# Optimization experiments

Measured on AMD Instinct MI355X. Metric: run time of the kernel, lower is better.

The kernel has to match this reference:

```python
import jax, jax.numpy as jnp
import numpy as np

E = 16        # n_routed_experts
D = 2048      # in_features
H = 1024      # d_intermediate per routed expert
K = 4         # n_activated_experts
SH = 1024     # shared expert hidden = n_shared_experts * d_intermediate
T = 2048      # tokens


def gated_mlp(x, w1, w2):
    # fc1 -> chunk -> y * silu(gate) -> fc2   (bias-free, as in mamba GatedMLP)
    y = x @ w1.T                      # [T, 2h]
    y, gate = jnp.split(y, 2, axis=-1)
    return (y * jax.nn.silu(gate)) @ w2.T


def setup_inputs() -> dict:
    key = jax.random.key(0)
    ks = jax.random.split(key, 6)
    s = 0.02  # init scale so softmax scores are well-behaved
    return {
        "x": jax.random.normal(ks[0], (T, D), jnp.float32),
        "gate_w": jax.random.normal(ks[1], (E, D), jnp.float32) * s,
        "w1": jax.random.normal(ks[2], (E, 2 * H, D), jnp.float32) * s,
        "w2": jax.random.normal(ks[3], (E, D, H), jnp.float32) * s,
        "sw1": jax.random.normal(ks[4], (2 * SH, D), jnp.float32) * s,
        "sw2": jax.random.normal(ks[5], (D, SH), jnp.float32) * s,
    }


def reference(x, gate_w, w1, w2, sw1, sw2):
    # ---- Gate (softmax scores in fp32, no bias, single expert group) ----
    scores = jax.nn.softmax((x @ gate_w.T).astype(jnp.float32), axis=-1)  # [T, E]
    top_vals, top_idx = jax.lax.top_k(scores, K)                          # [T, K]
    weights = top_vals.astype(x.dtype)  # route_scale = 1.0

    # Per-token routing weight per expert, [T, E]. topk indices are distinct
    # per token, matching `z[idx] += expert(x[idx]) * weights[idx, top]`.
    t_idx = jnp.arange(x.shape[0])[:, None]
    tok_w = jnp.zeros((x.shape[0], E), x.dtype).at[t_idx, top_idx].add(weights)

    # ---- Routed experts: accumulate weighted expert outputs ----
    def body(z, ew):
        w1_e, w2_e, we = ew  # [2H,D], [D,H], [T]
        return z + gated_mlp(x, w1_e, w2_e) * we[:, None], None

    z, _ = jax.lax.scan(body, jnp.zeros_like(x), (w1, w2, tok_w.T))

    # ---- Shared expert added to all tokens ----
    return z + gated_mlp(x, sw1, sw2)
```

## Files before the change

### kernel.cpp

```cpp
#include <hip/hip_runtime.h>
#include <stdint.h>

#define T_TOK 2048
#define D_IN  2048
#define H_I   1024
#define NE    16
#define TOPK  4
#define TWOH  2048
#define MAX_SLOTS 12288
#define MAX_TILES 96

typedef __attribute__((ext_vector_type(8))) __bf16 bf16x8;
typedef __attribute__((ext_vector_type(4))) float  f32x4;

__device__ __forceinline__ unsigned short f2bf(float f) {
  unsigned u = __float_as_uint(f);
  u += 0x7FFF + ((u >> 16) & 1);
  return (unsigned short)(u >> 16);
}
__device__ __forceinline__ float bf2f(unsigned short s) {
  return __uint_as_float(((unsigned)s) << 16);
}

__device__ __forceinline__ void group_meta(const int* __restrict__ cnt, int g,
                                           int& base, int& pc, int& shared_base) {
  int o = 0; base = 0; pc = T_TOK;
  for (int e = 0; e < NE; ++e) {
    int pce = (cnt[e] + 127) & ~127;
    if (e == g) { base = o; pc = pce; }
    o += pce;
  }
  shared_base = o;
  if (g == 16) base = o;
}

#define GLDS16(gp, lp) __builtin_amdgcn_global_load_lds( \
    (__attribute__((address_space(1))) void*)(gp),       \
    (__attribute__((address_space(3))) void*)(lp), 16, 0, 0)

#define R_X   1048576
#define R_W1  (R_X + 16777216)
#define R_W2  (R_W1 + 8388608)
#define R_SW1 (R_W2 + 1048576)
#define R_SW2 (R_SW1 + 524288)
__global__ void cvt_all(const float4* __restrict__ x,  const float4* __restrict__ w1,
                        const float4* __restrict__ w2, const float4* __restrict__ sw1,
                        const float4* __restrict__ sw2,
                        ushort4* __restrict__ xd,  ushort4* __restrict__ w1d,
                        ushort4* __restrict__ w2d, ushort4* __restrict__ sw1d,
                        ushort4* __restrict__ sw2d, int* __restrict__ cnt) {
  int i = blockIdx.x * 256 + threadIdx.x;
  if (i < NE) cnt[i] = 0;
  const float4* s; ushort4* d; int j;
  if      (i < R_X)   { s = x;   d = xd;   j = i; }
  else if (i < R_W1)  { s = w1;  d = w1d;  j = i - R_X; }
  else if (i < R_W2)  { s = w2;  d = w2d;  j = i - R_W1; }
  else if (i < R_SW1) { s = sw1; d = sw1d; j = i - R_W2; }
  else if (i < R_SW2) { s = sw2; d = sw2d; j = i - R_SW1; }
  else return;
  float4 f = s[j];
  ushort4 u;
  u.x = f2bf(f.x); u.y = f2bf(f.y); u.z = f2bf(f.z); u.w = f2bf(f.w);
  d[j] = u;
}

__global__ __launch_bounds__(256) void gate_topk(
    const float* __restrict__ x, const float* __restrict__ gw,
    int* __restrict__ cnt, int* __restrict__ cap_tok, float* __restrict__ cap_w,
    int* __restrict__ tk_ep)
{
  int t = blockIdx.x;
  const float* xr = x + (size_t)t * D_IN;
  float acc[NE];
#pragma unroll
  for (int e = 0; e < NE; ++e) acc[e] = 0.f;
  for (int d = threadIdx.x; d < D_IN; d += 256) {
    float xv = xr[d];
#pragma unroll
    for (int e = 0; e < NE; ++e) acc[e] += xv * gw[e * D_IN + d];
  }
#pragma unroll
  for (int e = 0; e < NE; ++e) {
    float v = acc[e];
#pragma unroll
    for (int o = 32; o > 0; o >>= 1) v += __shfl_down(v, o, 64);
    acc[e] = v;
  }
  __shared__ float red[4][NE];
  int wv = threadIdx.x >> 6, ln = threadIdx.x & 63;
  if (ln == 0) {
#pragma unroll
    for (int e = 0; e < NE; ++e) red[wv][e] = acc[e];
  }
  __syncthreads();
  if (threadIdx.x == 0) {
    float lg[NE];
    float mx = -1e30f;
#pragma unroll
    for (int e = 0; e < NE; ++e) {
      lg[e] = red[0][e] + red[1][e] + red[2][e] + red[3][e];
      mx = fmaxf(mx, lg[e]);
    }
    float s = 0.f;
#pragma unroll
    for (int e = 0; e < NE; ++e) { lg[e] = __expf(lg[e] - mx); s += lg[e]; }
    float inv = 1.f / s;
    bool used[NE] = {};
    for (int k = 0; k < TOPK; ++k) {
      float best = -1.f; int bi = 0;
      for (int e = 0; e < NE; ++e)
        if (!used[e] && lg[e] > best) { best = lg[e]; bi = e; }
      used[bi] = true;
      int pos = atomicAdd(&cnt[bi], 1);
      cap_tok[bi * T_TOK + pos] = t;
      cap_w[bi * T_TOK + pos]   = best * inv;
      tk_ep[t * TOPK + k] = (bi << 16) | pos;
    }
  }
}

__global__ void compact_lists(const int* __restrict__ cnt,
                              const int* __restrict__ cap_tok, const float* __restrict__ cap_w,
                              const int* __restrict__ tk_ep,
                              int* __restrict__ stok, float* __restrict__ swt,
                              int* __restrict__ tok2slot, int* __restrict__ tmap)
{
  int idx = blockIdx.x * 256 + threadIdx.x;
  if (idx == 0) {
    int k = 0, o = 0;
    for (int e = 0; e < NE; ++e) {
      int pce = (cnt[e] + 127) & ~127;
      for (int m = 0; m * 128 < pce && k < MAX_TILES; ++m)
        tmap[k++] = (e << 16) | (o + m * 128);
      o += pce;
    }
    for (int m = 0; m < 16 && k < MAX_TILES; ++m)
      tmap[k++] = (16 << 16) | (o + m * 128);
    tmap[MAX_TILES] = k;
  }
  if (idx < NE * T_TOK) {
    int e = idx >> 11, pos = idx & (T_TOK - 1);
    int base, pc, sb;
    group_meta(cnt, e, base, pc, sb);
    if (pos < pc) {
      int dst = base + pos;
      if (pos < cnt[e]) { stok[dst] = cap_tok[idx]; swt[dst] = cap_w[idx]; }
      else              { stok[dst] = 0;            swt[dst] = 0.f; }
    }
  } else if (idx < NE * T_TOK + T_TOK) {
    int t = idx - NE * T_TOK;
    int base, pc, sb;
    group_meta(cnt, 16, base, pc, sb);
    stok[base + t] = t; swt[base + t] = 1.f;
  } else {
    int j = idx - NE * T_TOK - T_TOK;
    int ep = tk_ep[j];
    int e = ep >> 16;
    int base, pc, sb;
    group_meta(cnt, e, base, pc, sb);
    tok2slot[j] = base + (ep & 0xFFFF);
  }
}

__global__ __launch_bounds__(256) void fc1_fused(
    const unsigned short* __restrict__ xbf,
    const unsigned short* __restrict__ w1bf,
    const unsigned short* __restrict__ sw1bf,
    const int* __restrict__ stok, const float* __restrict__ swt,
    const int* __restrict__ tmap,
    unsigned short* __restrict__ hbuf)
{
  int bx = blockIdx.x;
  int tile = bx >> 4, nt = bx & 15;
  if (tile >= tmap[MAX_TILES]) return;
  int tg = tmap[tile];
  int g = tg >> 16, base_slot = tg & 0xFFFF;
  const unsigned short* B = (g == 16) ? sw1bf : w1bf + (size_t)g * TWOH * D_IN;

  __shared__ __align__(16) unsigned char smem[32768];
  auto sA = (unsigned short (*)[64])smem;
  auto sB = (unsigned short (*)[64])(smem + 16384);
  auto sG = (float (*)[64])smem;

  int tid = threadIdx.x;
  int w = tid >> 6, l = tid & 63;
  int lm = l & 15, q = l >> 4;
  int wm = w >> 1, wn = w & 1;
  int r = l >> 3, c = l & 7;
  int csw = (c ^ r) << 3;

  const unsigned short* pA0 = xbf + (size_t)stok[base_slot + w * 32 +  0 + r] * D_IN + csw;
  const unsigned short* pA1 = xbf + (size_t)stok[base_slot + w * 32 +  8 + r] * D_IN + csw;
  const unsigned short* pA2 = xbf + (size_t)stok[base_slot + w * 32 + 16 + r] * D_IN + csw;
  const unsigned short* pA3 = xbf + (size_t)stok[base_slot + w * 32 + 24 + r] * D_IN + csw;
  int cb0 = w * 4;
  int br0 = (cb0 + 0 < 8) ? (nt * 64 + (cb0 + 0) * 8 + r) : (H_I + nt * 64 + (cb0 - 8) * 8 + r);
  int br1 = (cb0 + 1 < 8) ? (nt * 64 + (cb0 + 1) * 8 + r) : (H_I + nt * 64 + (cb0 - 7) * 8 + r);
  int br2 = (cb0 + 2 < 8) ? (nt * 64 + (cb0 + 2) * 8 + r) : (H_I + nt * 64 + (cb0 - 6) * 8 + r);
  int br3 = (cb0 + 3 < 8) ? (nt * 64 + (cb0 + 3) * 8 + r) : (H_I + nt * 64 + (cb0 - 5) * 8 + r);
  const unsigned short* pB0 = B + (size_t)br0 * D_IN + csw;
  const unsigned short* pB1 = B + (size_t)br1 * D_IN + csw;
  const unsigned short* pB2 = B + (size_t)br2 * D_IN + csw;
  const unsigned short* pB3 = B + (size_t)br3 * D_IN + csw;

  f32x4 acc[4][4];
#pragma unroll
  for (int i = 0; i < 4; ++i)
#pragma unroll
    for (int j = 0; j < 4; ++j) acc[i][j] = (f32x4){0.f, 0.f, 0.f, 0.f};

  for (int kt = 0; kt < D_IN; kt += 64) {
    GLDS16(pA0 + kt, &sA[w * 32 +  0][0]);
    GLDS16(pA1 + kt, &sA[w * 32 +  8][0]);
    GLDS16(pA2 + kt, &sA[w * 32 + 16][0]);
    GLDS16(pA3 + kt, &sA[w * 32 + 24][0]);
    GLDS16(pB0 + kt, &sB[w * 32 +  0][0]);
    GLDS16(pB1 + kt, &sB[w * 32 +  8][0]);
    GLDS16(pB2 + kt, &sB[w * 32 + 16][0]);
    GLDS16(pB3 + kt, &sB[w * 32 + 24][0]);
    __syncthreads();
    bf16x8 af[2][4], bfr[2][4];
#pragma unroll
    for (int s = 0; s < 2; ++s) {
#pragma unroll
      for (int i = 0; i < 4; ++i) {
        int row = wm * 64 + i * 16 + lm;
        af[s][i] = *(const bf16x8*)&sA[row][(((s << 2) + q) ^ (lm & 7)) << 3];
      }
#pragma unroll
      for (int j = 0; j < 4; ++j) {
        int row = wn * 64 + j * 16 + lm;
        bfr[s][j] = *(const bf16x8*)&sB[row][(((s << 2) + q) ^ (lm & 7)) << 3];
      }
    }
#pragma unroll
    for (int s = 0; s < 2; ++s)
#pragma unroll
      for (int i = 0; i < 4; ++i)
#pragma unroll
        for (int j = 0; j < 4; ++j)
          acc[i][j] = __builtin_amdgcn_mfma_f32_16x16x32_bf16(af[s][i], bfr[s][j], acc[i][j], 0, 0, 0);
    __syncthreads();
  }

  if (wn == 1) {
#pragma unroll
    for (int i = 0; i < 4; ++i)
#pragma unroll
      for (int rr = 0; rr < 4; ++rr) {
        int row = wm * 64 + i * 16 + q * 4 + rr;
        int sw = (row & 3) << 4;
#pragma unroll
        for (int j = 0; j < 4; ++j) {
          float gv = acc[i][j][rr];
          sG[row][(j * 16 + lm) ^ sw] = gv / (1.f + __expf(-gv));
        }
      }
  }
  __syncthreads();
  if (wn == 0) {
#pragma unroll
    for (int i = 0; i < 4; ++i)
#pragma unroll
      for (int rr = 0; rr < 4; ++rr) {
        int row = wm * 64 + i * 16 + q * 4 + rr;
        int slot = base_slot + row;
        float wt = swt[slot];
        int sw = (row & 3) << 4;
        unsigned short* hrow = hbuf + (size_t)slot * H_I + nt * 64;
#pragma unroll
        for (int j = 0; j < 4; ++j) {
          int col = j * 16 + lm;
          hrow[col] = f2bf(acc[i][j][rr] * sG[row][col ^ sw] * wt);
        }
      }
  }
}

__global__ __launch_bounds__(256) void fc2_gemm(
    const unsigned short* __restrict__ hbuf,
    const unsigned short* __restrict__ w2bf,
    const unsigned short* __restrict__ sw2bf,
    const int* __restrict__ tmap,
    unsigned short* __restrict__ Yout)
{
  int bx = blockIdx.x;
  int tile = bx >> 4, nt = bx & 15;
  if (tile >= tmap[MAX_TILES]) return;
  int tg = tmap[tile];
  int g = tg >> 16, base_slot = tg & 0xFFFF;
  const unsigned short* B = (g == 16) ? sw2bf : w2bf + (size_t)g * D_IN * H_I;

  __shared__ __align__(16) unsigned char smem[32768];
  auto sA = (unsigned short (*)[64])smem;
  auto sB = (unsigned short (*)[64])(smem + 16384);

  int tid = threadIdx.x;
  int w = tid >> 6, l = tid & 63;
  int lm = l & 15, q = l >> 4;
  int wm = w >> 1, wn = w & 1;
  int r = l >> 3, c = l & 7;
  int csw = (c ^ r) << 3;

  const unsigned short* pA0 = hbuf + (size_t)(base_slot + w * 32 +  0 + r) * H_I + csw;
  const unsigned short* pA1 = hbuf + (size_t)(base_slot + w * 32 +  8 + r) * H_I + csw;
  const unsigned short* pA2 = hbuf + (size_t)(base_slot + w * 32 + 16 + r) * H_I + csw;
  const unsigned short* pA3 = hbuf + (size_t)(base_slot + w * 32 + 24 + r) * H_I + csw;
  const unsigned short* pB0 = B + (size_t)(nt * 128 + w * 32 +  0 + r) * H_I + csw;
  const unsigned short* pB1 = B + (size_t)(nt * 128 + w * 32 +  8 + r) * H_I + csw;
  const unsigned short* pB2 = B + (size_t)(nt * 128 + w * 32 + 16 + r) * H_I + csw;
  const unsigned short* pB3 = B + (size_t)(nt * 128 + w * 32 + 24 + r) * H_I + csw;

  f32x4 acc[4][4];
#pragma unroll
  for (int i = 0; i < 4; ++i)
#pragma unroll
    for (int j = 0; j < 4; ++j) acc[i][j] = (f32x4){0.f, 0.f, 0.f, 0.f};

  for (int kt = 0; kt < H_I; kt += 64) {
    GLDS16(pA0 + kt, &sA[w * 32 +  0][0]);
    GLDS16(pA1 + kt, &sA[w * 32 +  8][0]);
    GLDS16(pA2 + kt, &sA[w * 32 + 16][0]);
    GLDS16(pA3 + kt, &sA[w * 32 + 24][0]);
    GLDS16(pB0 + kt, &sB[w * 32 +  0][0]);
    GLDS16(pB1 + kt, &sB[w * 32 +  8][0]);
    GLDS16(pB2 + kt, &sB[w * 32 + 16][0]);
    GLDS16(pB3 + kt, &sB[w * 32 + 24][0]);
    __syncthreads();
    bf16x8 af[2][4], bfr[2][4];
#pragma unroll
    for (int s = 0; s < 2; ++s) {
#pragma unroll
      for (int i = 0; i < 4; ++i) {
        int row = wm * 64 + i * 16 + lm;
        af[s][i] = *(const bf16x8*)&sA[row][(((s << 2) + q) ^ (lm & 7)) << 3];
      }
#pragma unroll
      for (int j = 0; j < 4; ++j) {
        int row = wn * 64 + j * 16 + lm;
        bfr[s][j] = *(const bf16x8*)&sB[row][(((s << 2) + q) ^ (lm & 7)) << 3];
      }
    }
#pragma unroll
    for (int s = 0; s < 2; ++s)
#pragma unroll
      for (int i = 0; i < 4; ++i)
#pragma unroll
        for (int j = 0; j < 4; ++j)
          acc[i][j] = __builtin_amdgcn_mfma_f32_16x16x32_bf16(af[s][i], bfr[s][j], acc[i][j], 0, 0, 0);
    __syncthreads();
  }

  int colbase = nt * 128 + wn * 64;
#pragma unroll
  for (int i = 0; i < 4; ++i) {
#pragma unroll
    for (int rr = 0; rr < 4; ++rr) {
      int row = wm * 64 + i * 16 + q * 4 + rr;
      unsigned short* orow = Yout + (size_t)(base_slot + row) * D_IN + colbase + lm;
#pragma unroll
      for (int j = 0; j < 4; ++j)
        orow[j * 16] = f2bf(acc[i][j][rr]);
    }
  }
}

__global__ __launch_bounds__(256) void reduce_out(
    const unsigned short* __restrict__ Yout, const int* __restrict__ tok2slot,
    const int* __restrict__ cnt, float4* __restrict__ out)
{
  int idx = blockIdx.x * 256 + threadIdx.x;
  int t = idx >> 9, c = (idx & 511) << 2;
  int sb = 0;
  for (int e = 0; e < NE; ++e) sb += (cnt[e] + 127) & ~127;
  int sl[5];
  sl[0] = sb + t;
#pragma unroll
  for (int k = 0; k < TOPK; ++k) sl[k + 1] = tok2slot[t * TOPK + k];
  float4 a = {0.f, 0.f, 0.f, 0.f};
#pragma unroll
  for (int k = 0; k < 5; ++k) {
    ushort4 v = *(const ushort4*)(Yout + (size_t)sl[k] * D_IN + c);
    a.x += bf2f(v.x); a.y += bf2f(v.y); a.z += bf2f(v.z); a.w += bf2f(v.w);
  }
  out[idx] = a;
}

extern "C" void kernel_launch(void* const* d_in, const int* in_sizes, int n_in,
                              void* d_out, int out_size, void* d_ws, size_t ws_size,
                              hipStream_t stream)
{
  const float* x   = (const float*)d_in[0];
  const float* gw  = (const float*)d_in[1];
  const float* w1  = (const float*)d_in[2];
  const float* w2  = (const float*)d_in[3];
  const float* sw1 = (const float*)d_in[4];
  const float* sw2 = (const float*)d_in[5];
  float* out = (float*)d_out;

  char* ws = (char*)d_ws;
  size_t off = 0;
  auto alloc = [&](size_t bytes) -> char* {
    char* p = ws + off; off += (bytes + 255) & ~(size_t)255; return p;
  };
  unsigned short* xbf   = (unsigned short*)alloc((size_t)T_TOK * D_IN * 2);
  unsigned short* w1bf  = (unsigned short*)alloc((size_t)NE * TWOH * D_IN * 2);
  unsigned short* w2bf  = (unsigned short*)alloc((size_t)NE * D_IN * H_I * 2);
  unsigned short* sw1bf = (unsigned short*)alloc((size_t)TWOH * D_IN * 2);
  unsigned short* sw2bf = (unsigned short*)alloc((size_t)D_IN * H_I * 2);
  unsigned short* hbuf  = (unsigned short*)alloc((size_t)MAX_SLOTS * H_I * 2);
  int*   cnt    = (int*)alloc(NE * 4);
  int*   captok = (int*)alloc((size_t)NE * T_TOK * 4);
  float* capw   = (float*)alloc((size_t)NE * T_TOK * 4);
  int*   stok   = (int*)alloc(MAX_SLOTS * 4);
  float* swt    = (float*)alloc(MAX_SLOTS * 4);
  int*   tk_ep  = (int*)alloc((size_t)T_TOK * TOPK * 4);
  int*   t2s    = (int*)alloc((size_t)T_TOK * TOPK * 4);
  int*   tmap   = (int*)alloc((MAX_TILES + 1) * 4);
  if (off > ws_size) return;

  unsigned short* Yout = (unsigned short*)w1bf;

  cvt_all<<<(R_SW2 + 255) / 256, 256, 0, stream>>>(
      (const float4*)x, (const float4*)w1, (const float4*)w2,
      (const float4*)sw1, (const float4*)sw2,
      (ushort4*)xbf, (ushort4*)w1bf, (ushort4*)w2bf, (ushort4*)sw1bf, (ushort4*)sw2bf, cnt);

  gate_topk<<<T_TOK, 256, 0, stream>>>(x, gw, cnt, captok, capw, tk_ep);
  compact_lists<<<(NE * T_TOK + T_TOK + TOPK * T_TOK) / 256, 256, 0, stream>>>(
      cnt, captok, capw, tk_ep, stok, swt, t2s, tmap);
  fc1_fused<<<MAX_TILES * 16, 256, 0, stream>>>(xbf, w1bf, sw1bf, stok, swt, tmap, hbuf);
  fc2_gemm<<<MAX_TILES * 16, 256, 0, stream>>>(hbuf, w2bf, sw2bf, tmap, Yout);
  reduce_out<<<(T_TOK * 512) / 256, 256, 0, stream>>>(Yout, t2s, cnt, (float4*)out);
}
```

Measured before the change: 794.4 us.

## Double-buffer LDS tiles in fc1 and fc2 GEMM main loops

Both grouped GEMM kernels now keep two LDS stages. Each iteration issues the global-to-LDS loads for the next K tile before computing on the current one, with one barrier per iteration instead of two. The goal is to hide global load latency behind MFMA work. Doubling shared memory to 64KB per block may lower the number of resident blocks per CU. The raw s_waitcnt plus s_barrier sequence also assumes the LDS reads are complete before the buffer is overwritten.

```diff
diff --git a/kernel.cpp b/kernel.cpp
--- a/kernel.cpp
+++ b/kernel.cpp
@@ -177,9 +177,7 @@
   int g = tg >> 16, base_slot = tg & 0xFFFF;
   const unsigned short* B = (g == 16) ? sw1bf : w1bf + (size_t)g * TWOH * D_IN;
 
-  __shared__ __align__(16) unsigned char smem[32768];
-  auto sA = (unsigned short (*)[64])smem;
-  auto sB = (unsigned short (*)[64])(smem + 16384);
+  __shared__ __align__(16) unsigned char smem[65536];
   auto sG = (float (*)[64])smem;
 
   int tid = threadIdx.x;
@@ -209,39 +207,59 @@
 #pragma unroll
     for (int j = 0; j < 4; ++j) acc[i][j] = (f32x4){0.f, 0.f, 0.f, 0.f};
 
+#define STAGE_FC1(BUF, KT) do {                                          \
+    unsigned char* b_ = smem + ((BUF) << 15);                            \
+    auto sA_ = (unsigned short (*)[64])b_;                               \
+    auto sB_ = (unsigned short (*)[64])(b_ + 16384);                     \
+    GLDS16(pA0 + (KT), &sA_[w * 32 +  0][0]);                            \
+    GLDS16(pA1 + (KT), &sA_[w * 32 +  8][0]);                            \
+    GLDS16(pA2 + (KT), &sA_[w * 32 + 16][0]);                            \
+    GLDS16(pA3 + (KT), &sA_[w * 32 + 24][0]);                            \
+    GLDS16(pB0 + (KT), &sB_[w * 32 +  0][0]);                            \
+    GLDS16(pB1 + (KT), &sB_[w * 32 +  8][0]);                            \
+    GLDS16(pB2 + (KT), &sB_[w * 32 + 16][0]);                            \
+    GLDS16(pB3 + (KT), &sB_[w * 32 + 24][0]);                            \
+  } while (0)
+
+#define COMPUTE_FC1(BUF) do {                                            \
+    unsigned char* b_ = smem + ((BUF) << 15);                            \
+    auto sA_ = (unsigned short (*)[64])b_;                               \
+    auto sB_ = (unsigned short (*)[64])(b_ + 16384);                     \
+    bf16x8 af[2][4], bfr[2][4];                                          \
+    _Pragma("unroll")                                                    \
+    for (int s = 0; s < 2; ++s) {                                        \
+      _Pragma("unroll")                                                  \
+      for (int i = 0; i < 4; ++i) {                                      \
+        int row = wm * 64 + i * 16 + lm;                                 \
+        af[s][i] = *(const bf16x8*)&sA_[row][(((s << 2) + q) ^ (lm & 7)) << 3]; \
+      }                                                                  \
+      _Pragma("unroll")                                                  \
+      for (int j = 0; j < 4; ++j) {                                      \
+        int row = wn * 64 + j * 16 + lm;                                 \
+        bfr[s][j] = *(const bf16x8*)&sB_[row][(((s << 2) + q) ^ (lm & 7)) << 3]; \
+      }                                                                  \
+    }                                                                    \
+    _Pragma("unroll")                                                    \
+    for (int s = 0; s < 2; ++s)                                          \
+      _Pragma("unroll")                                                  \
+      for (int i = 0; i < 4; ++i)                                        \
+        _Pragma("unroll")                                                \
+        for (int j = 0; j < 4; ++j)                                      \
+          acc[i][j] = __builtin_amdgcn_mfma_f32_16x16x32_bf16(af[s][i], bfr[s][j], acc[i][j], 0, 0, 0); \
+  } while (0)
+
+  STAGE_FC1(0, 0);
+  asm volatile("s_waitcnt vmcnt(0)" ::: "memory");
+  __builtin_amdgcn_s_barrier();
   for (int kt = 0; kt < D_IN; kt += 64) {
-    GLDS16(pA0 + kt, &sA[w * 32 +  0][0]);
-    GLDS16(pA1 + kt, &sA[w * 32 +  8][0]);
-    GLDS16(pA2 + kt, &sA[w * 32 + 16][0]);
-    GLDS16(pA3 + kt, &sA[w * 32 + 24][0]);
-    GLDS16(pB0 + kt, &sB[w * 32 +  0][0]);
-    GLDS16(pB1 + kt, &sB[w * 32 +  8][0]);
-    GLDS16(pB2 + kt, &sB[w * 32 + 16][0]);
-    GLDS16(pB3 + kt, &sB[w * 32 + 24][0]);
-    __syncthreads();
-    bf16x8 af[2][4], bfr[2][4];
-#pragma unroll
-    for (int s = 0; s < 2; ++s) {
-#pragma unroll
-      for (int i = 0; i < 4; ++i) {
-        int row = wm * 64 + i * 16 + lm;
-        af[s][i] = *(const bf16x8*)&sA[row][(((s << 2) + q) ^ (lm & 7)) << 3];
-      }
-#pragma unroll
-      for (int j = 0; j < 4; ++j) {
-        int row = wn * 64 + j * 16 + lm;
-        bfr[s][j] = *(const bf16x8*)&sB[row][(((s << 2) + q) ^ (lm & 7)) << 3];
-      }
-    }
-#pragma unroll
-    for (int s = 0; s < 2; ++s)
-#pragma unroll
-      for (int i = 0; i < 4; ++i)
-#pragma unroll
-        for (int j = 0; j < 4; ++j)
-          acc[i][j] = __builtin_amdgcn_mfma_f32_16x16x32_bf16(af[s][i], bfr[s][j], acc[i][j], 0, 0, 0);
-    __syncthreads();
-  }
+    int cur = (kt >> 6) & 1;
+    if (kt + 64 < D_IN) STAGE_FC1(cur ^ 1, kt + 64);
+    COMPUTE_FC1(cur);
+    asm volatile("s_waitcnt vmcnt(0)" ::: "memory");
+    __builtin_amdgcn_s_barrier();
+  }
+#undef STAGE_FC1
+#undef COMPUTE_FC1
 
   if (wn == 1) {
 #pragma unroll
@@ -291,9 +309,7 @@
   int g = tg >> 16, base_slot = tg & 0xFFFF;
   const unsigned short* B = (g == 16) ? sw2bf : w2bf + (size_t)g * D_IN * H_I;
 
-  __shared__ __align__(16) unsigned char smem[32768];
-  auto sA = (unsigned short (*)[64])smem;
-  auto sB = (unsigned short (*)[64])(smem + 16384);
+  __shared__ __align__(16) unsigned char smem[65536];
 
   int tid = threadIdx.x;
   int w = tid >> 6, l = tid & 63;
@@ -317,39 +333,59 @@
 #pragma unroll
     for (int j = 0; j < 4; ++j) acc[i][j] = (f32x4){0.f, 0.f, 0.f, 0.f};
 
+#define STAGE_FC2(BUF, KT) do {                                          \
+    unsigned char* b_ = smem + ((BUF) << 15);                            \
+    auto sA_ = (unsigned short (*)[64])b_;                               \
+    auto sB_ = (unsigned short (*)[64])(b_ + 16384);                     \
+    GLDS16(pA0 + (KT), &sA_[w * 32 +  0][0]);                            \
+    GLDS16(pA1 + (KT), &sA_[w * 32 +  8][0]);                            \
+    GLDS16(pA2 + (KT), &sA_[w * 32 + 16][0]);                            \
+    GLDS16(pA3 + (KT), &sA_[w * 32 + 24][0]);                            \
+    GLDS16(pB0 + (KT), &sB_[w * 32 +  0][0]);                            \
+    GLDS16(pB1 + (KT), &sB_[w * 32 +  8][0]);                            \
+    GLDS16(pB2 + (KT), &sB_[w * 32 + 16][0]);                            \
+    GLDS16(pB3 + (KT), &sB_[w * 32 + 24][0]);                            \
+  } while (0)
+
+#define COMPUTE_FC2(BUF) do {                                            \
+    unsigned char* b_ = smem + ((BUF) << 15);                            \
+    auto sA_ = (unsigned short (*)[64])b_;                               \
+    auto sB_ = (unsigned short (*)[64])(b_ + 16384);                     \
+    bf16x8 af[2][4], bfr[2][4];                                          \
+    _Pragma("unroll")                                                    \
+    for (int s = 0; s < 2; ++s) {                                        \
+      _Pragma("unroll")                                                  \
+      for (int i = 0; i < 4; ++i) {                                      \
+        int row = wm * 64 + i * 16 + lm;                                 \
+        af[s][i] = *(const bf16x8*)&sA_[row][(((s << 2) + q) ^ (lm & 7)) << 3]; \
+      }                                                                  \
+      _Pragma("unroll")                                                  \
+      for (int j = 0; j < 4; ++j) {                                      \
+        int row = wn * 64 + j * 16 + lm;                                 \
+        bfr[s][j] = *(const bf16x8*)&sB_[row][(((s << 2) + q) ^ (lm & 7)) << 3]; \
+      }                                                                  \
+    }                                                                    \
+    _Pragma("unroll")                                                    \
+    for (int s = 0; s < 2; ++s)                                          \
+      _Pragma("unroll")                                                  \
+      for (int i = 0; i < 4; ++i)                                        \
+        _Pragma("unroll")                                                \
+        for (int j = 0; j < 4; ++j)                                      \
+          acc[i][j] = __builtin_amdgcn_mfma_f32_16x16x32_bf16(af[s][i], bfr[s][j], acc[i][j], 0, 0, 0); \
+  } while (0)
+
+  STAGE_FC2(0, 0);
+  asm volatile("s_waitcnt vmcnt(0)" ::: "memory");
+  __builtin_amdgcn_s_barrier();
   for (int kt = 0; kt < H_I; kt += 64) {
-    GLDS16(pA0 + kt, &sA[w * 32 +  0][0]);
-    GLDS16(pA1 + kt, &sA[w * 32 +  8][0]);
-    GLDS16(pA2 + kt, &sA[w * 32 + 16][0]);
-    GLDS16(pA3 + kt, &sA[w * 32 + 24][0]);
-    GLDS16(pB0 + kt, &sB[w * 32 +  0][0]);
-    GLDS16(pB1 + kt, &sB[w * 32 +  8][0]);
-    GLDS16(pB2 + kt, &sB[w * 32 + 16][0]);
-    GLDS16(pB3 + kt, &sB[w * 32 + 24][0]);
-    __syncthreads();
-    bf16x8 af[2][4], bfr[2][4];
-#pragma unroll
-    for (int s = 0; s < 2; ++s) {
-#pragma unroll
-      for (int i = 0; i < 4; ++i) {
-        int row = wm * 64 + i * 16 + lm;
-        af[s][i] = *(const bf16x8*)&sA[row][(((s << 2) + q) ^ (lm & 7)) << 3];
-      }
-#pragma unroll
-      for (int j = 0; j < 4; ++j) {
-        int row = wn * 64 + j * 16 + lm;
-        bfr[s][j] = *(const bf16x8*)&sB[row][(((s << 2) + q) ^ (lm & 7)) << 3];
-      }
-    }
-#pragma unroll
-    for (int s = 0; s < 2; ++s)
-#pragma unroll
-      for (int i = 0; i < 4; ++i)
-#pragma unroll
-        for (int j = 0; j < 4; ++j)
-          acc[i][j] = __builtin_amdgcn_mfma_f32_16x16x32_bf16(af[s][i], bfr[s][j], acc[i][j], 0, 0, 0);
-    __syncthreads();
-  }
+    int cur = (kt >> 6) & 1;
+    if (kt + 64 < H_I) STAGE_FC2(cur ^ 1, kt + 64);
+    COMPUTE_FC2(cur);
+    asm volatile("s_waitcnt vmcnt(0)" ::: "memory");
+    __builtin_amdgcn_s_barrier();
+  }
+#undef STAGE_FC2
+#undef COMPUTE_FC2
 
   int colbase = nt * 128 + wn * 64;
 #pragma unroll
```

Measured after the change: 785.8 us. About the same (-1.1%).
